# Kernel optimization log

Measured on AMD Instinct MI355X. Metric: run time of the kernel, lower is better.

## Reference

```python
import jax, jax.numpy as jnp
import numpy as np

T = 131072      # timesteps
F = 8           # features per timestep; close price at column 3
HIDDEN = 256
MAX_K = 10
BUF = 50        # sliding buffer size


def _hfd_all(p):
    """Higuchi fractal dimension over a trailing window of BUF prices, for every t.

    Replicates: buffer grows to BUF then slides; HFD computed only once
    len(buffer) > MAX_K, else 0. p: [T] float.
    """
    Tn = p.shape[0]
    t = jnp.arange(Tn)
    n = jnp.minimum(t + 1, BUF)                 # buffer length at step t
    nm1 = n - 1
    nm1f = nm1.astype(p.dtype)
    starts = jnp.maximum(0, t + 1 - BUF)
    idx = jnp.clip(starts[:, None] + jnp.arange(BUF)[None, :], 0, Tn - 1)
    W = p[idx]                                   # [T, BUF] left-aligned windows

    lk_cols = []
    for k in range(1, MAX_K + 1):
        # lag-k abs diffs within each window: D[t, q] = |W[t, q+k] - W[t, q]|
        D = jnp.abs(W[:, k:] - W[:, :-k])        # [T, BUF-k]
        pos = jnp.arange(BUF - k)
        D = jnp.where(pos[None, :] + k <= nm1[:, None], D, jnp.zeros((), p.dtype))
        acc = jnp.zeros(Tn, p.dtype)
        for m in range(k):
            pm = np.arange(m, BUF - k, k)        # positions m, m+k, ... in D
            S = D[:, pm].sum(axis=1)             # sum of |arr[m+(j+1)k]-arr[m+jk]|
            length = jnp.where(nm1 >= m, (nm1 - m) // k + 1, 0)  # len(idxs)
            good = length >= 2
            lf = jnp.maximum(length, 1).astype(p.dtype)
            acc = acc + jnp.where(good, S * nm1f / (lf * k), jnp.zeros((), p.dtype))
        lk_cols.append(acc / k)
    Lk = jnp.stack(lk_cols, axis=1)              # [T, MAX_K]

    # log-log linear fit (polyfit deg 1) over k with Lk > 0
    logk = jnp.log(jnp.arange(1, MAX_K + 1, dtype=p.dtype))
    valid = Lk > 0
    wv = valid.astype(p.dtype)
    loglk = jnp.where(valid, jnp.log(jnp.where(valid, Lk, jnp.ones((), p.dtype))), jnp.zeros((), p.dtype))
    c = wv.sum(1)
    sx = (wv * logk).sum(1)
    sy = loglk.sum(1)
    sxy = (loglk * logk).sum(1)
    sxx = (wv * logk * logk).sum(1)
    denom = c * sxx - sx * sx
    safe = jnp.where(denom != 0, denom, jnp.ones((), p.dtype))
    slope = (c * sxy - sx * sy) / safe
    hfd = -slope
    return jnp.where((c > 1) & (n >= MAX_K + 1), hfd, jnp.zeros((), p.dtype))


def setup_inputs() -> dict:
    key = jax.random.key(0)
    k1, k2, k3 = jax.random.split(key, 3)
    x = jax.random.normal(k1, (T, F), jnp.float32)
    w_lin = jax.random.normal(k2, (HIDDEN, 1), jnp.float32) * 0.1   # nn.Linear(1, hidden)
    b_lin = jax.random.normal(k3, (HIDDEN,), jnp.float32) * 0.1
    return {"x": x, "w_lin": w_lin, "b_lin": b_lin}


def reference(x, w_lin, b_lin):
    hfd = _hfd_all(x[:, 3])                      # [T]
    # relu(linear(hfd[:, None])) with in_features=1
    return jax.nn.relu(hfd[:, None] * w_lin[:, 0][None, :] + b_lin[None, :])
```

## Files before the change

kernel.cpp:

```cpp
#include <hip/hip_runtime.h>
#include <math.h>

#define T_TOTAL 131072
#define FEAT    8
#define HIDDEN  256
#define MAXK    10
#define BUF     50
#define BT      256

__device__ __forceinline__ float fit_loglog(const float Lk[MAXK]) {
    const float logk[MAXK] = {0.0f,        0.6931472f, 1.0986123f, 1.3862944f,
                              1.6094379f,  1.7917595f, 1.9459101f, 2.0794415f,
                              2.1972246f,  2.3025851f};
    float c = 0.f, sx = 0.f, sy = 0.f, sxy = 0.f, sxx = 0.f;
#pragma unroll
    for (int i = 0; i < MAXK; ++i) {
        if (Lk[i] > 0.0f) {
            const float lx = logk[i];
            const float ly = logf(Lk[i]);
            c   += 1.0f;
            sx  += lx;
            sy  += ly;
            sxy += ly * lx;
            sxx += lx * lx;
        }
    }
    float denom = c * sxx - sx * sx;
    denom = (denom != 0.0f) ? denom : 1.0f;
    const float slope = (c * sxy - sx * sy) / denom;
    return (c > 1.0f) ? -slope : 0.0f;
}

__global__ __launch_bounds__(BT) void hfd_fused(const float* __restrict__ x,
                                                const float* __restrict__ w_lin,
                                                const float* __restrict__ b_lin,
                                                float* __restrict__ out) {
    __shared__ float sp[BT + BUF - 1];
    __shared__ float shfd[BT];

    const int tid = threadIdx.x;
    const int t0  = blockIdx.x * BT;

    for (int i = tid; i < BT + BUF - 1; i += BT) {
        const int gt = t0 - (BUF - 1) + i;
        sp[i] = (gt >= 0) ? x[(size_t)gt * FEAT + 3] : 0.0f;
    }
    __syncthreads();

    const int t = t0 + tid;
    float hfd = 0.0f;

    if (t >= BUF - 1) {
        float w[BUF];
#pragma unroll
        for (int q = 0; q < BUF; ++q) w[q] = sp[tid + q];

        float Lk[MAXK];
#pragma unroll
        for (int k = 1; k <= MAXK; ++k) {
            float acc = 0.0f;
#pragma unroll
            for (int m = 0; m < k; ++m) {
                float S = 0.0f;
#pragma unroll
                for (int q = m; q + k <= BUF - 1; q += k)
                    S += fabsf(w[q + k] - w[q]);
                const int len = (BUF - 1 - m) / k + 1;
                acc += S * ((float)(BUF - 1) / (float)(len * k));
            }
            Lk[k - 1] = acc / (float)k;
        }
        hfd = fit_loglog(Lk);
    } else if (t >= MAXK) {
        const int   nm1  = t;
        const float nm1f = (float)nm1;
        const float* wp  = &sp[BUF - 1];

        float Lk[MAXK];
        for (int k = 1; k <= MAXK; ++k) {
            float acc = 0.0f;
            for (int m = 0; m < k; ++m) {
                float S = 0.0f;
                for (int q = m; q + k <= nm1; q += k)
                    S += fabsf(wp[q + k] - wp[q]);
                const int length = (nm1 >= m) ? ((nm1 - m) / k + 1) : 0;
                if (length >= 2)
                    acc += S * nm1f / (float)(length * k);
            }
            Lk[k - 1] = acc / (float)k;
        }
        hfd = fit_loglog(Lk);
    }

    shfd[tid] = hfd;
    __syncthreads();

    const int hg = tid & 63;
    const int r0 = tid >> 6;
    const float4 wv = ((const float4*)w_lin)[hg];
    const float4 bv = ((const float4*)b_lin)[hg];
    float4* outv = (float4*)out;

#pragma unroll 4
    for (int r = r0; r < BT; r += 4) {
        const float h = shfd[r];
        float4 o;
        o.x = fmaxf(fmaf(h, wv.x, bv.x), 0.0f);
        o.y = fmaxf(fmaf(h, wv.y, bv.y), 0.0f);
        o.z = fmaxf(fmaf(h, wv.z, bv.z), 0.0f);
        o.w = fmaxf(fmaf(h, wv.w, bv.w), 0.0f);
        outv[(size_t)(t0 + r) * (HIDDEN / 4) + hg] = o;
    }
}

extern "C" void kernel_launch(void* const* d_in, const int* in_sizes, int n_in,
                              void* d_out, int out_size, void* d_ws, size_t ws_size,
                              hipStream_t stream) {
    const float* x     = (const float*)d_in[0];
    const float* w_lin = (const float*)d_in[1];
    const float* b_lin = (const float*)d_in[2];
    float* out = (float*)d_out;

    const int nblocks = T_TOTAL / BT;
    hfd_fused<<<dim3(nblocks), dim3(BT), 0, stream>>>(x, w_lin, b_lin, out);
}
```

Baseline: 164.8 us.

## Split fused HFD kernel into compute and wide-grid output expansion kernels

Separates the HFD computation from the linear+ReLU output expansion into two kernels, passing per-timestep HFD values through workspace memory. The expansion kernel uses small 64-row blocks, giving a much larger grid so the write-bound output stores are spread across more workgroups. The aim is to decouple the compute-heavy phase from the bandwidth-heavy phase. In exchange it adds a second launch and a round trip through global memory for the HFD values.

After: 170.3 us. 3.3% more time.

```diff
diff --git a/kernel.cpp b/kernel.cpp
--- a/kernel.cpp
+++ b/kernel.cpp
@@ -7,6 +7,7 @@
 #define MAXK    10
 #define BUF     50
 #define BT      256
+#define ROWS    64
 
 __device__ __forceinline__ float fit_loglog(const float Lk[MAXK]) {
     const float logk[MAXK] = {0.0f,        0.6931472f, 1.0986123f, 1.3862944f,
@@ -31,12 +32,9 @@
     return (c > 1.0f) ? -slope : 0.0f;
 }
 
-__global__ __launch_bounds__(BT) void hfd_fused(const float* __restrict__ x,
-                                                const float* __restrict__ w_lin,
-                                                const float* __restrict__ b_lin,
-                                                float* __restrict__ out) {
+__global__ __launch_bounds__(BT) void hfd_compute(const float* __restrict__ x,
+                                                  float* __restrict__ hfd_out) {
     __shared__ float sp[BT + BUF - 1];
-    __shared__ float shfd[BT];
 
     const int tid = threadIdx.x;
     const int t0  = blockIdx.x * BT;
@@ -92,18 +90,29 @@
         hfd = fit_loglog(Lk);
     }
 
-    shfd[tid] = hfd;
+    hfd_out[t] = hfd;
+}
+
+__global__ __launch_bounds__(256) void expand_out(const float* __restrict__ hfd,
+                                                  const float* __restrict__ w_lin,
+                                                  const float* __restrict__ b_lin,
+                                                  float4* __restrict__ outv) {
+    __shared__ float sh[ROWS];
+    const int tid = threadIdx.x;
+    const int t0  = blockIdx.x * ROWS;
+
+    if (tid < ROWS) sh[tid] = hfd[t0 + tid];
+
+    const int hg = tid & 63;
+    const int ph = tid >> 6;
+    const float4 wv = ((const float4*)w_lin)[hg];
+    const float4 bv = ((const float4*)b_lin)[hg];
     __syncthreads();
 
-    const int hg = tid & 63;
-    const int r0 = tid >> 6;
-    const float4 wv = ((const float4*)w_lin)[hg];
-    const float4 bv = ((const float4*)b_lin)[hg];
-    float4* outv = (float4*)out;
-
-#pragma unroll 4
-    for (int r = r0; r < BT; r += 4) {
-        const float h = shfd[r];
+#pragma unroll
+    for (int i = 0; i < ROWS / 4; ++i) {
+        const int r = 4 * i + ph;
+        const float h = sh[r];
         float4 o;
         o.x = fmaxf(fmaf(h, wv.x, bv.x), 0.0f);
         o.y = fmaxf(fmaf(h, wv.y, bv.y), 0.0f);
@@ -120,7 +129,9 @@
     const float* w_lin = (const float*)d_in[1];
     const float* b_lin = (const float*)d_in[2];
     float* out = (float*)d_out;
+    float* hfd = (float*)d_ws;
 
-    const int nblocks = T_TOTAL / BT;
-    hfd_fused<<<dim3(nblocks), dim3(BT), 0, stream>>>(x, w_lin, b_lin, out);
+    hfd_compute<<<dim3(T_TOTAL / BT), dim3(BT), 0, stream>>>(x, hfd);
+    expand_out<<<dim3(T_TOTAL / ROWS), dim3(256), 0, stream>>>(
+        hfd, w_lin, b_lin, (float4*)out);
 }
```
